# Optimization experiments

Measured on AMD Instinct MI355X. Metric: run time of the kernel, lower is better.

The kernel has to match this reference:

```python
import jax, jax.numpy as jnp
import numpy as np

B, E, T = 2, 512, 2048
H = 8
LOCAL_SIZE = 128
NEG_INF = -1e9


def setup_inputs() -> dict:
    key = jax.random.key(0)
    ks = jax.random.split(key, 5)
    return {
        "x": jax.random.normal(ks[0], (B, E, T), dtype=jnp.float32),
        "in_proj_w": jax.random.normal(ks[1], (3 * E, E), dtype=jnp.float32) * (E ** -0.5),
        "in_proj_b": jax.random.normal(ks[2], (3 * E,), dtype=jnp.float32) * 0.02,
        "out_w": jax.random.normal(ks[3], (E, E), dtype=jnp.float32) * (E ** -0.5),
        "out_b": jax.random.normal(ks[4], (E,), dtype=jnp.float32) * 0.02,
    }


def _local_mask(t, local_size, dtype):
    # allowed iff |i - j| <= local_size // 2 (sliding local window)
    i = jnp.arange(t)[:, None]
    j = jnp.arange(t)[None, :]
    allowed = jnp.abs(i - j) <= (local_size // 2)
    return jnp.where(allowed, jnp.zeros((), dtype), jnp.full((), NEG_INF, dtype))


def reference(x, in_proj_w, in_proj_b, out_w, out_b):
    dh = E // H
    scale = 1.0 / jnp.sqrt(jnp.asarray(dh, x.dtype))
    xt = jnp.transpose(x, (0, 2, 1))               # [B, T, E]
    qkv = xt @ in_proj_w.T + in_proj_b             # [B, T, 3E]
    q, k, v = jnp.split(qkv, 3, axis=-1)
    q = q.reshape(B, T, H, dh)
    k = k.reshape(B, T, H, dh)
    v = v.reshape(B, T, H, dh)
    scores = jnp.einsum("bqhd,bkhd->bhqk", q, k) * scale  # [B, H, T, T]
    scores = scores + _local_mask(T, LOCAL_SIZE, scores.dtype)
    attn = jax.nn.softmax(scores, axis=-1)
    ctx = jnp.einsum("bhqk,bkhd->bqhd", attn, v).reshape(B, T, E)
    attn_out = ctx @ out_w.T + out_b               # [B, T, E]
    attn_out = jnp.transpose(attn_out, (0, 2, 1))  # [B, E, T]
    return jax.nn.relu(attn_out * x)
```

## Files before the change

kernel.cpp:

```cpp
#include <hip/hip_runtime.h>
#include <stdint.h>


#define DEVI __device__ __forceinline__

typedef __attribute__((ext_vector_type(8))) short bf16x8;
typedef __attribute__((ext_vector_type(4))) float f32x4;

DEVI unsigned short f2bf(float f) {
  unsigned u = __float_as_uint(f);
  u += 0x7fffu + ((u >> 16) & 1u);
  return (unsigned short)(u >> 16);
}
DEVI float bf2f(unsigned short h) { return __uint_as_float(((unsigned)h) << 16); }

#define GLL16(gp, lp)                                                          \
  __builtin_amdgcn_global_load_lds(                                            \
      (const __attribute__((address_space(1))) void*)(gp),                     \
      (__attribute__((address_space(3))) void*)(lp), 16, 0, 0)

#define MFMA(a, b, c) __builtin_amdgcn_mfma_f32_16x16x32_bf16((a), (b), (c), 0, 0, 0)

__global__ __launch_bounds__(256) void k_prep(
    const float* __restrict__ x, const float* __restrict__ w_in,
    const float* __restrict__ w_out, unsigned short* __restrict__ xh,
    unsigned short* __restrict__ wih, unsigned short* __restrict__ woh) {
  const int tid = threadIdx.x;
  if (blockIdx.y == 8) {
    int cb = (blockIdx.z << 5) | blockIdx.x;
    const float* src;
    unsigned short* dst;
    int base;
    if (cb < 48) {
      src = w_in; dst = wih; base = cb * 16384;
    } else {
      src = w_out; dst = woh; base = (cb - 48) * 16384;
    }
#pragma unroll
    for (int k = 0; k < 16; k++) {
      int idx = base + (k * 256 + tid) * 4;
      float4 v = *(const float4*)&src[idx];
      ushort4 o;
      o.x = f2bf(v.x); o.y = f2bf(v.y); o.z = f2bf(v.z); o.w = f2bf(v.w);
      *(ushort4*)&dst[idx] = o;
    }
    return;
  }
  __shared__ float tile[64][65];
  const int b = blockIdx.z, e0 = blockIdx.y * 64, t0 = blockIdx.x * 64;
  const int g = tid >> 4, c4 = (tid & 15) * 4;
#pragma unroll
  for (int p = 0; p < 4; p++) {
    int el = p * 16 + g;
    float4 v = *(const float4*)&x[((size_t)b * 512 + e0 + el) * 2048 + t0 + c4];
    tile[el][c4 + 0] = v.x; tile[el][c4 + 1] = v.y;
    tile[el][c4 + 2] = v.z; tile[el][c4 + 3] = v.w;
  }
  __syncthreads();
#pragma unroll
  for (int p = 0; p < 4; p++) {
    int tl = p * 16 + g;
    ushort4 o;
    o.x = f2bf(tile[c4 + 0][tl]);
    o.y = f2bf(tile[c4 + 1][tl]);
    o.z = f2bf(tile[c4 + 2][tl]);
    o.w = f2bf(tile[c4 + 3][tl]);
    *(ushort4*)&xh[((size_t)(b * 2048 + t0 + tl)) * 512 + e0 + c4] = o;
  }
}

__global__ __launch_bounds__(256) void k_gemm_qkv(
    const unsigned short* __restrict__ Ahg, const unsigned short* __restrict__ Bhg,
    const float* __restrict__ bias, unsigned short* __restrict__ Qs,
    unsigned short* __restrict__ Kks, unsigned short* __restrict__ VvT) {
  const int KD = 512;
  __shared__ __align__(16) unsigned short Ah_s[128 * 32];
  __shared__ __align__(16) unsigned short Bh_s[128 * 32];
  const int tid = threadIdx.x, lane = tid & 63, w = tid >> 6;
  const int bid = blockIdx.x;
  const int xcd = bid & 7, j5 = bid >> 3;
  const int m0 = (xcd * 4 + j5 / 12) * 128, n0 = (j5 % 12) * 128;
  const int wm = (w >> 1) * 64, wn = (w & 1) * 64;

  f32x4 acc[4][4];
#pragma unroll
  for (int i = 0; i < 4; i++)
#pragma unroll
    for (int j = 0; j < 4; j++) acc[i][j] = (f32x4){0.f, 0.f, 0.f, 0.f};

  const int srw = lane >> 2, sc = (lane & 3) * 8;
  const size_t b0 = (size_t)(n0 + w * 32 + srw) * KD + sc;
  const size_t b1 = b0 + (size_t)16 * KD;
  unsigned short* lB0 = &Bh_s[(w * 32) * 32];
  unsigned short* lB1 = &Bh_s[(w * 32 + 16) * 32];
  const size_t a0 = (size_t)(m0 + w * 32 + srw) * KD + sc;
  const size_t a1 = a0 + (size_t)16 * KD;
  unsigned short* lAh0 = &Ah_s[(w * 32) * 32];
  unsigned short* lAh1 = &Ah_s[(w * 32 + 16) * 32];

  const int fm = lane & 15, fq = (lane >> 4) * 8;

  for (int k0 = 0; k0 < KD; k0 += 32) {
    __syncthreads();
    GLL16(Ahg + a0 + k0, lAh0);
    GLL16(Ahg + a1 + k0, lAh1);
    GLL16(Bhg + b0 + k0, lB0);
    GLL16(Bhg + b1 + k0, lB1);
    __builtin_amdgcn_s_waitcnt(0);
    __syncthreads();

    bf16x8 ah[4], bh[4];
#pragma unroll
    for (int i = 0; i < 4; i++) {
      ah[i] = *(const bf16x8*)&Ah_s[(wm + i * 16 + fm) * 32 + fq];
      bh[i] = *(const bf16x8*)&Bh_s[(wn + i * 16 + fm) * 32 + fq];
    }
#pragma unroll
    for (int i = 0; i < 4; i++)
#pragma unroll
      for (int j = 0; j < 4; j++)
        acc[i][j] = MFMA(ah[i], bh[j], acc[i][j]);
  }

  const int quad = lane >> 4;
#pragma unroll
  for (int i = 0; i < 4; i++)
#pragma unroll
    for (int j = 0; j < 4; j++) {
      int gn = n0 + wn + j * 16 + fm;
      float bv = bias[gn];
      int sec = gn >> 9, cc = gn & 511;
      int h = cc >> 6, d = cc & 63;
      int gm0 = m0 + wm + i * 16 + quad * 4;
      int bb = gm0 >> 11, t = gm0 & 2047;
      if (sec == 2) {
        ushort4 pk;
        pk.x = f2bf(acc[i][j][0] + bv);
        pk.y = f2bf(acc[i][j][1] + bv);
        pk.z = f2bf(acc[i][j][2] + bv);
        pk.w = f2bf(acc[i][j][3] + bv);
        *(ushort4*)&VvT[(((size_t)(bb * 8 + h)) * 64 + d) * 2048 + t] = pk;
      } else {
        unsigned short* dst = sec == 0 ? Qs : Kks;
        float mul = sec == 0 ? 0.125f : 1.0f;
#pragma unroll
        for (int r = 0; r < 4; r++) {
          float v = (acc[i][j][r] + bv) * mul;
          dst[(((size_t)(bb * 8 + h)) * 2048 + t + r) * 64 + d] = f2bf(v);
        }
      }
    }
}

__global__ __launch_bounds__(256) void k_gemm_out(
    const unsigned short* __restrict__ Ahg, const unsigned short* __restrict__ Bhg,
    const float* __restrict__ bias, const float* __restrict__ x,
    float* __restrict__ out) {
  const int KD = 512;
  __shared__ __align__(16) union {
    struct {
      unsigned short Ah[64 * 32];
      unsigned short Bh[128 * 32];
    } st;
    float tile[64][129];
  } u;
  const int tid = threadIdx.x, lane = tid & 63, w = tid >> 6;
  const int bid = blockIdx.x;
  const int xcd = bid & 7, j5 = bid >> 3;
  const int m0 = (xcd * 8 + (j5 >> 2)) * 64, n0 = (j5 & 3) * 128;
  const int wm = (w >> 1) * 32, wn = (w & 1) * 64;

  f32x4 acc[2][4];
#pragma unroll
  for (int i = 0; i < 2; i++)
#pragma unroll
    for (int j = 0; j < 4; j++) acc[i][j] = (f32x4){0.f, 0.f, 0.f, 0.f};

  const int srw = lane >> 2, sc = (lane & 3) * 8;
  const size_t b0 = (size_t)(n0 + w * 32 + srw) * KD + sc;
  const size_t b1 = b0 + (size_t)16 * KD;
  const size_t a0 = (size_t)(m0 + w * 16 + srw) * KD + sc;
  unsigned short* lB0 = &u.st.Bh[(w * 32) * 32];
  unsigned short* lB1 = &u.st.Bh[(w * 32 + 16) * 32];
  unsigned short* lAh0 = &u.st.Ah[(w * 16) * 32];

  const int fm = lane & 15, fq = (lane >> 4) * 8;

  for (int k0 = 0; k0 < KD; k0 += 32) {
    __syncthreads();
    GLL16(Ahg + a0 + k0, lAh0);
    GLL16(Bhg + b0 + k0, lB0);
    GLL16(Bhg + b1 + k0, lB1);
    __builtin_amdgcn_s_waitcnt(0);
    __syncthreads();

    bf16x8 ah[2], bh[4];
#pragma unroll
    for (int i = 0; i < 2; i++)
      ah[i] = *(const bf16x8*)&u.st.Ah[(wm + i * 16 + fm) * 32 + fq];
#pragma unroll
    for (int j = 0; j < 4; j++)
      bh[j] = *(const bf16x8*)&u.st.Bh[(wn + j * 16 + fm) * 32 + fq];
#pragma unroll
    for (int i = 0; i < 2; i++)
#pragma unroll
      for (int j = 0; j < 4; j++)
        acc[i][j] = MFMA(ah[i], bh[j], acc[i][j]);
  }

  __syncthreads();
  const int quad = lane >> 4;
#pragma unroll
  for (int i = 0; i < 2; i++)
#pragma unroll
    for (int j = 0; j < 4; j++) {
      int ln = wn + j * 16 + fm;
      float bv = bias[n0 + ln];
#pragma unroll
      for (int r = 0; r < 4; r++) {
        int lm = wm + i * 16 + quad * 4 + r;
        u.tile[lm][ln] = acc[i][j][r] + bv;
      }
    }
  __syncthreads();

  const int bb = m0 >> 11, t0 = m0 & 2047;
  const int tt = tid & 63, e0w = tid >> 6;
#pragma unroll
  for (int k = 0; k < 32; k++) {
    int ee = e0w + k * 4;
    size_t o = ((size_t)bb * 512 + n0 + ee) * 2048 + t0 + tt;
    float v = u.tile[tt][ee] * x[o];
    out[o] = fmaxf(v, 0.f);
  }
}

#define PSTR 200
__global__ __launch_bounds__(256, 4) void k_attention(
    const unsigned short* __restrict__ Qs, const unsigned short* __restrict__ Kks,
    const unsigned short* __restrict__ VvT, unsigned short* __restrict__ ctx_hi) {
  __shared__ __align__(16) unsigned short P_s[64 * PSTR];

  const int tid = threadIdx.x, lane = tid & 63, w = tid >> 6;
  const int q0 = blockIdx.x * 64;
  const int bh = blockIdx.y;
  const int j0 = q0 - 64;
  const size_t base = (size_t)bh * 2048 * 64;
  const int fm = lane & 15, quad = lane >> 4;

  bf16x8 aq[2];
  {
    const size_t qb = base + (size_t)(q0 + w * 16 + fm) * 64 + quad * 8;
#pragma unroll
    for (int ks = 0; ks < 2; ks++)
      aq[ks] = *(const bf16x8*)&Qs[qb + ks * 32];
  }

  const int ct0 = (w >> 1) * 2;
  f32x4 sa[10];
#pragma unroll
  for (int u2 = 0; u2 < 10; u2++) sa[u2] = (f32x4){0.f, 0.f, 0.f, 0.f};
  __builtin_amdgcn_s_setprio(1);
#pragma unroll
  for (int u2 = 0; u2 < 10; u2++) {
    int jr = j0 + (ct0 + u2) * 16 + fm;
    jr = jr < 0 ? 0 : (jr > 2047 ? 2047 : jr);
    const unsigned short* kp = &Kks[base + (size_t)jr * 64 + quad * 8];
#pragma unroll
    for (int ks = 0; ks < 2; ks++) {
      bf16x8 bk = *(const bf16x8*)&kp[ks * 32];
      sa[u2] = MFMA(aq[ks], bk, sa[u2]);
    }
  }
  __builtin_amdgcn_s_setprio(0);

  float rm[4], rs[4], inv[4];
#pragma unroll
  for (int r = 0; r < 4; r++) rm[r] = -1e30f;
#pragma unroll
  for (int u2 = 0; u2 < 10; u2++) {
    int jj = (ct0 + u2) * 16 + fm;
    int jg = j0 + jj;
    bool jok = (jg >= 0) && (jg < 2048);
#pragma unroll
    for (int r = 0; r < 4; r++) {
      int ii = w * 16 + quad * 4 + r;
      bool ok = jok && (jj >= ii) && (jj <= ii + 128);
      float sv = ok ? sa[u2][r] : -1e30f;
      sa[u2][r] = sv;
      rm[r] = fmaxf(rm[r], sv);
    }
  }
#pragma unroll
  for (int off = 1; off < 16; off <<= 1)
#pragma unroll
    for (int r = 0; r < 4; r++) rm[r] = fmaxf(rm[r], __shfl_xor(rm[r], off));
#pragma unroll
  for (int r = 0; r < 4; r++) rs[r] = 0.f;
#pragma unroll
  for (int u2 = 0; u2 < 10; u2++)
#pragma unroll
    for (int r = 0; r < 4; r++) {
      float e = __expf(sa[u2][r] - rm[r]);
      sa[u2][r] = e;
      rs[r] += e;
    }
#pragma unroll
  for (int off = 1; off < 16; off <<= 1)
#pragma unroll
    for (int r = 0; r < 4; r++) rs[r] += __shfl_xor(rs[r], off);
#pragma unroll
  for (int r = 0; r < 4; r++) inv[r] = 1.0f / rs[r];

#pragma unroll
  for (int u2 = 0; u2 < 10; u2++)
#pragma unroll
    for (int r = 0; r < 4; r++) {
      int row = w * 16 + quad * 4 + r;
      P_s[row * PSTR + (ct0 + u2) * 16 + fm] = f2bf(sa[u2][r] * inv[r]);
    }
  asm volatile("s_waitcnt lgkmcnt(0)" ::: "memory");
  __builtin_amdgcn_sched_barrier(0);

  const int ks0 = w >> 1;
  f32x4 oa[4];
#pragma unroll
  for (int dt = 0; dt < 4; dt++) oa[dt] = (f32x4){0.f, 0.f, 0.f, 0.f};
  __builtin_amdgcn_s_setprio(1);
#pragma unroll
  for (int ku = 0; ku < 5; ku++) {
    int ks = ks0 + ku;
    bf16x8 ap = *(const bf16x8*)&P_s[(w * 16 + fm) * PSTR + ks * 32 + quad * 8];
    int j = j0 + ks * 32 + quad * 8;
    j = (j < 0 || j > 2040) ? 0 : j;
    const unsigned short* vp = &VvT[base + j];
#pragma unroll
    for (int dt = 0; dt < 4; dt++) {
      bf16x8 bv = *(const bf16x8*)&vp[(size_t)(dt * 16 + fm) * 2048];
      oa[dt] = MFMA(ap, bv, oa[dt]);
    }
  }
  __builtin_amdgcn_s_setprio(0);

  const int bb = bh >> 3, h = bh & 7;
#pragma unroll
  for (int dt = 0; dt < 4; dt++)
#pragma unroll
    for (int r = 0; r < 4; r++) {
      int t = q0 + w * 16 + quad * 4 + r;
      int c = h * 64 + dt * 16 + fm;
      ctx_hi[((size_t)(bb * 2048 + t)) * 512 + c] = f2bf(oa[dt][r]);
    }
}

extern "C" void kernel_launch(void* const* d_in, const int* in_sizes, int n_in,
                              void* d_out, int out_size, void* d_ws, size_t ws_size,
                              hipStream_t stream) {
  const float* x = (const float*)d_in[0];
  const float* w_in = (const float*)d_in[1];
  const float* b_in = (const float*)d_in[2];
  const float* w_out = (const float*)d_in[3];
  const float* b_out = (const float*)d_in[4];
  float* out = (float*)d_out;

  uint8_t* ws = (uint8_t*)d_ws;
  unsigned short* xT_hi = (unsigned short*)(ws + 0);
  unsigned short* wih   = (unsigned short*)(ws + 8388608);
  unsigned short* woh   = (unsigned short*)(ws + 9961472);
  unsigned short* Qs    = (unsigned short*)(ws + 12582912);
  unsigned short* Kk    = (unsigned short*)(ws + 16777216);
  unsigned short* VvT   = (unsigned short*)(ws + 20971520);
  unsigned short* ctxh  = (unsigned short*)(ws + 25165824);

  k_prep<<<dim3(32, 9, 2), 256, 0, stream>>>(x, w_in, w_out, xT_hi, wih, woh);
  k_gemm_qkv<<<384, 256, 0, stream>>>(xT_hi, wih, b_in, Qs, Kk, VvT);
  k_attention<<<dim3(32, 16), 256, 0, stream>>>(Qs, Kk, VvT, ctxh);
  k_gemm_out<<<256, 256, 0, stream>>>(ctxh, woh, b_out, x, out);
}
```

Baseline: 115.3 us.

## Double-buffer LDS tiles in QKV and output projection GEMMs

Both projection GEMMs now keep two LDS buffers for A and B. The next K-slice is issued with global_load_lds while MFMAs run on the current one, replacing the old load, wait, compute sequence. The explicit waitcnt is removed, so correctness relies on __syncthreads draining the outstanding direct-to-LDS loads. LDS use per block doubles for the staging buffers, which may reduce occupancy slightly.

```diff
diff --git a/kernel.cpp b/kernel.cpp
--- a/kernel.cpp
+++ b/kernel.cpp
@@ -74,8 +74,8 @@
     const float* __restrict__ bias, unsigned short* __restrict__ Qs,
     unsigned short* __restrict__ Kks, unsigned short* __restrict__ VvT) {
   const int KD = 512;
-  __shared__ __align__(16) unsigned short Ah_s[128 * 32];
-  __shared__ __align__(16) unsigned short Bh_s[128 * 32];
+  __shared__ __align__(16) unsigned short Ah_s[2 * 128 * 32];
+  __shared__ __align__(16) unsigned short Bh_s[2 * 128 * 32];
   const int tid = threadIdx.x, lane = tid & 63, w = tid >> 6;
   const int bid = blockIdx.x;
   const int xcd = bid & 7, j5 = bid >> 3;
@@ -91,35 +91,47 @@
   const int srw = lane >> 2, sc = (lane & 3) * 8;
   const size_t b0 = (size_t)(n0 + w * 32 + srw) * KD + sc;
   const size_t b1 = b0 + (size_t)16 * KD;
-  unsigned short* lB0 = &Bh_s[(w * 32) * 32];
-  unsigned short* lB1 = &Bh_s[(w * 32 + 16) * 32];
   const size_t a0 = (size_t)(m0 + w * 32 + srw) * KD + sc;
   const size_t a1 = a0 + (size_t)16 * KD;
-  unsigned short* lAh0 = &Ah_s[(w * 32) * 32];
-  unsigned short* lAh1 = &Ah_s[(w * 32 + 16) * 32];
+
+  unsigned short* A0 = Ah_s;
+  unsigned short* A1 = Ah_s + 128 * 32;
+  unsigned short* B0 = Bh_s;
+  unsigned short* B1 = Bh_s + 128 * 32;
 
   const int fm = lane & 15, fq = (lane >> 4) * 8;
-
-  for (int k0 = 0; k0 < KD; k0 += 32) {
-    __syncthreads();
-    GLL16(Ahg + a0 + k0, lAh0);
-    GLL16(Ahg + a1 + k0, lAh1);
-    GLL16(Bhg + b0 + k0, lB0);
-    GLL16(Bhg + b1 + k0, lB1);
-    __builtin_amdgcn_s_waitcnt(0);
-    __syncthreads();
-
+  const int lA0 = (w * 32) * 32, lA1 = (w * 32 + 16) * 32;
+
+  auto stage = [&](int kk, unsigned short* A, unsigned short* B) {
+    GLL16(Ahg + a0 + kk, A + lA0);
+    GLL16(Ahg + a1 + kk, A + lA1);
+    GLL16(Bhg + b0 + kk, B + lA0);
+    GLL16(Bhg + b1 + kk, B + lA1);
+  };
+  auto compute = [&](const unsigned short* A, const unsigned short* B) {
     bf16x8 ah[4], bh[4];
 #pragma unroll
     for (int i = 0; i < 4; i++) {
-      ah[i] = *(const bf16x8*)&Ah_s[(wm + i * 16 + fm) * 32 + fq];
-      bh[i] = *(const bf16x8*)&Bh_s[(wn + i * 16 + fm) * 32 + fq];
+      ah[i] = *(const bf16x8*)&A[(wm + i * 16 + fm) * 32 + fq];
+      bh[i] = *(const bf16x8*)&B[(wn + i * 16 + fm) * 32 + fq];
     }
 #pragma unroll
     for (int i = 0; i < 4; i++)
 #pragma unroll
       for (int j = 0; j < 4; j++)
         acc[i][j] = MFMA(ah[i], bh[j], acc[i][j]);
+  };
+
+  stage(0, A0, B0);
+  __syncthreads();
+#pragma unroll
+  for (int k0 = 0; k0 < KD; k0 += 64) {
+    if (k0 + 32 < KD) stage(k0 + 32, A1, B1);
+    compute(A0, B0);
+    __syncthreads();
+    if (k0 + 64 < KD) stage(k0 + 64, A0, B0);
+    compute(A1, B1);
+    __syncthreads();
   }
 
   const int quad = lane >> 4;
@@ -159,8 +171,8 @@
   const int KD = 512;
   __shared__ __align__(16) union {
     struct {
-      unsigned short Ah[64 * 32];
-      unsigned short Bh[128 * 32];
+      unsigned short Ah[2 * 64 * 32];
+      unsigned short Bh[2 * 128 * 32];
     } st;
     float tile[64][129];
   } u;
@@ -180,35 +192,48 @@
   const size_t b0 = (size_t)(n0 + w * 32 + srw) * KD + sc;
   const size_t b1 = b0 + (size_t)16 * KD;
   const size_t a0 = (size_t)(m0 + w * 16 + srw) * KD + sc;
-  unsigned short* lB0 = &u.st.Bh[(w * 32) * 32];
-  unsigned short* lB1 = &u.st.Bh[(w * 32 + 16) * 32];
-  unsigned short* lAh0 = &u.st.Ah[(w * 16) * 32];
+
+  unsigned short* A0 = u.st.Ah;
+  unsigned short* A1 = u.st.Ah + 64 * 32;
+  unsigned short* B0 = u.st.Bh;
+  unsigned short* B1 = u.st.Bh + 128 * 32;
 
   const int fm = lane & 15, fq = (lane >> 4) * 8;
-
-  for (int k0 = 0; k0 < KD; k0 += 32) {
-    __syncthreads();
-    GLL16(Ahg + a0 + k0, lAh0);
-    GLL16(Bhg + b0 + k0, lB0);
-    GLL16(Bhg + b1 + k0, lB1);
-    __builtin_amdgcn_s_waitcnt(0);
-    __syncthreads();
-
+  const int lB0 = (w * 32) * 32, lB1 = (w * 32 + 16) * 32;
+  const int lA0 = (w * 16) * 32;
+
+  auto stage = [&](int kk, unsigned short* A, unsigned short* B) {
+    GLL16(Ahg + a0 + kk, A + lA0);
+    GLL16(Bhg + b0 + kk, B + lB0);
+    GLL16(Bhg + b1 + kk, B + lB1);
+  };
+  auto compute = [&](const unsigned short* A, const unsigned short* B) {
     bf16x8 ah[2], bh[4];
 #pragma unroll
     for (int i = 0; i < 2; i++)
-      ah[i] = *(const bf16x8*)&u.st.Ah[(wm + i * 16 + fm) * 32 + fq];
+      ah[i] = *(const bf16x8*)&A[(wm + i * 16 + fm) * 32 + fq];
 #pragma unroll
     for (int j = 0; j < 4; j++)
-      bh[j] = *(const bf16x8*)&u.st.Bh[(wn + j * 16 + fm) * 32 + fq];
+      bh[j] = *(const bf16x8*)&B[(wn + j * 16 + fm) * 32 + fq];
 #pragma unroll
     for (int i = 0; i < 2; i++)
 #pragma unroll
       for (int j = 0; j < 4; j++)
         acc[i][j] = MFMA(ah[i], bh[j], acc[i][j]);
-  }
-
+  };
+
+  stage(0, A0, B0);
   __syncthreads();
+#pragma unroll
+  for (int k0 = 0; k0 < KD; k0 += 64) {
+    if (k0 + 32 < KD) stage(k0 + 32, A1, B1);
+    compute(A0, B0);
+    __syncthreads();
+    if (k0 + 64 < KD) stage(k0 + 64, A0, B0);
+    compute(A1, B1);
+    __syncthreads();
+  }
+
   const int quad = lane >> 4;
 #pragma unroll
   for (int i = 0; i < 2; i++)
```

After: 114.2 us. No clear change (-0.9%).
